# Kernel tuning notes

Measured on AMD Instinct MI355X. Metric: run time of the kernel, lower is better.

Reference implementation:

```python
import jax, jax.numpy as jnp
import numpy as np

EPS = 1e-8  # matches F.cosine_similarity default eps


def setup_inputs() -> dict:
    key = jax.random.key(0)
    k1, k2, k3 = jax.random.split(key, 3)
    B, C, H, W = 16, 256, 64, 64
    n_e = 1024
    z = jax.random.normal(k1, (B, C, H, W), dtype=jnp.float32)
    gt = jax.random.normal(k2, (B, C, H, W), dtype=jnp.float32)
    codebook = jax.random.normal(k3, (n_e, C), dtype=jnp.float32)
    return {"z": z, "gt": gt, "codebook": codebook}


def _sq_dist(x, cb):
    return (jnp.sum(x * x, axis=1, keepdims=True)
            + jnp.sum(cb * cb, axis=1)
            - 2.0 * x @ cb.T)


def reference(z, gt, codebook):
    B, C, H, W = z.shape
    # permute to (B,H,W,C) then flatten to (N, e_dim)
    zf = jnp.transpose(z, (0, 2, 3, 1)).reshape(-1, C)
    gf = jnp.transpose(gt, (0, 2, 3, 1)).reshape(-1, C)

    idx = jnp.argmin(_sq_dist(zf, codebook), axis=1)       # [N]
    idx_gt = jnp.argmin(_sq_dist(gf, codebook), axis=1)    # [N]

    # one-hot @ codebook == direct gather
    z_q = codebook[idx].reshape(B, H, W, C)
    z_q_gt = codebook[idx_gt].reshape(B, H, W, C)

    # F.cosine_similarity(z_q_gt, z_q, dim=1) on (B,H,W,C): reduces over H -> (B,W,C)
    num = jnp.sum(z_q_gt * z_q, axis=1)
    nx = jnp.maximum(jnp.sqrt(jnp.sum(z_q_gt * z_q_gt, axis=1)), EPS)
    ny = jnp.maximum(jnp.sqrt(jnp.sum(z_q * z_q, axis=1)), EPS)
    cosine_score = num / (nx * ny)                         # (B, W, C)

    return cosine_score, idx_gt[:, None], idx[:, None]
```

## Files before the change

### kernel.cpp

```cpp
#include <hip/hip_runtime.h>

typedef _Float16 f16x8 __attribute__((ext_vector_type(8)));
typedef float f32x16 __attribute__((ext_vector_type(16)));

#define CDIM 256
#define NE 1024
#define HW 4096
#define CHW 1048576
#define OUT_COS 262144
#define N_PIX 65536
#define NT 32
#define TAU 0.1f


__global__ void prep_kernel(const float* __restrict__ cb,
                            _Float16* __restrict__ hi,
                            float* __restrict__ c2f,
                            double* __restrict__ c2d) {
    int code = blockIdx.x;
    int lane = threadIdx.x;
    int t = code >> 5, n = code & 31;
    const float* row = cb + code * CDIM;
    double s = 0.0;
    #pragma unroll
    for (int i = 0; i < 4; ++i) {
        int d = i * 64 + lane;
        float x = row[d];
        s += (double)x * (double)x;
        int f = d >> 4, q = (d >> 3) & 1, rr = d & 7;
        hi[(size_t)t * 8192 + f * 512 + q * 256 + n * 8 + rr] = (_Float16)x;
    }
    #pragma unroll
    for (int off = 32; off > 0; off >>= 1)
        s += __shfl_down(s, off, 64);
    if (lane == 0) { c2f[code] = (float)(0.5 * s); c2d[code] = 0.5 * s; }
}

__device__ __forceinline__ void gl_lds16(const _Float16* g, _Float16* l) {
    __builtin_amdgcn_global_load_lds(
        (const __attribute__((address_space(1))) unsigned int*)g,
        (__attribute__((address_space(3))) unsigned int*)l, 16, 0, 0);
}

__launch_bounds__(256, 2)
__global__ void argmin_kernel(const float* __restrict__ Z,
                              const float* __restrict__ GT,
                              const _Float16* __restrict__ ghi,
                              const float* __restrict__ cb,
                              const float* __restrict__ c2f,
                              const double* __restrict__ c2d,
                              float* __restrict__ out_z,
                              float* __restrict__ out_gt) {
    __shared__ __align__(16) _Float16 lbuf[2][8192];
    __shared__ int cand_lds[4][64];
    const int wave = threadIdx.x >> 6;
    const int lane = threadIdx.x & 63;
    const int l31 = lane & 31;
    const int qh = lane >> 5;
    const int half = blockIdx.x >> 8;
    const float* X = half ? GT : Z;
    float* out_idx = half ? out_gt : out_z;
    const int p0 = (blockIdx.x & 255) * 256;

    f16x8 nah[2][16];
    #pragma unroll
    for (int g = 0; g < 2; ++g) {
        const int p = p0 + wave * 64 + g * 32 + l31;
        const float* xbase = X + (size_t)(p >> 12) * CHW + (p & 4095);
        #pragma unroll
        for (int f = 0; f < 16; ++f) {
            #pragma unroll
            for (int j = 0; j < 8; ++j) {
                int d = f * 16 + qh * 8 + j;
                nah[g][f][j] = -(_Float16)xbase[(size_t)d * HW];
            }
        }
    }

    int b1[2][16], b2[2][16];
    #pragma unroll
    for (int g = 0; g < 2; ++g)
        #pragma unroll
        for (int r = 0; r < 16; ++r) { b1[g][r] = 0x7fffffff; b2[g][r] = 0x7fffffff; }

    auto stage = [&](int b, int t) {
        #pragma unroll
        for (int i = 0; i < 4; ++i) {
            const int f = wave * 4 + i;
            gl_lds16(ghi + (size_t)t * 8192 + f * 512 + lane * 8, &lbuf[b][f * 512]);
        }
    };

    stage(0, 0);
    __syncthreads();

    for (int t = 0; t < NT; ++t) {
        const int cur = t & 1;
        if (t < NT - 1) stage(cur ^ 1, t + 1);

        const float c2 = c2f[t * 32 + l31];
        f32x16 acc0, acc1;
        #pragma unroll
        for (int r = 0; r < 16; ++r) { acc0[r] = c2; acc1[r] = c2; }

        #pragma unroll
        for (int f = 0; f < 16; ++f) {
            f16x8 bh = *(const f16x8*)&lbuf[cur][f * 512 + lane * 8];
            acc0 = __builtin_amdgcn_mfma_f32_32x32x16_f16(nah[0][f], bh, acc0, 0, 0, 0);
            acc1 = __builtin_amdgcn_mfma_f32_32x32x16_f16(nah[1][f], bh, acc1, 0, 0, 0);
        }

        const int n = t * 32 + l31;
        #pragma unroll
        for (int r = 0; r < 16; ++r) {
            int k0 = (__float_as_int(acc0[r]) & 0xFFFFFC00) | n;
            int t0 = max(b1[0][r], k0);
            b2[0][r] = min(b2[0][r], t0);
            b1[0][r] = min(b1[0][r], k0);
            int k1 = (__float_as_int(acc1[r]) & 0xFFFFFC00) | n;
            int t1 = max(b1[1][r], k1);
            b2[1][r] = min(b2[1][r], t1);
            b1[1][r] = min(b1[1][r], k1);
        }
        __syncthreads();
    }

    #pragma unroll
    for (int g = 0; g < 2; ++g) {
        #pragma unroll
        for (int r = 0; r < 16; ++r) {
            int x1 = b1[g][r], x2 = b2[g][r];
            #pragma unroll
            for (int off = 16; off > 0; off >>= 1) {
                int o1 = __shfl_xor(x1, off, 64);
                int o2 = __shfl_xor(x2, off, 64);
                int tt = max(x1, o1);
                x2 = min(min(x2, o2), tt);
                x1 = min(x1, o1);
            }
            if (l31 == 0) {
                const int i1 = x1 & 1023, i2 = x2 & 1023;
                const float s1 = __int_as_float(x1 & 0xFFFFFC00);
                const float s2 = __int_as_float(x2 & 0xFFFFFC00);
                const int row = (r & 3) + 8 * (r >> 2) + 4 * qh;
                const int slot = g * 32 + row;
                const bool flag = (s2 - s1) < TAU;
                cand_lds[wave][slot] = i1 | (i2 << 10) | (flag ? (1 << 20) : 0);
                if (!flag) out_idx[p0 + wave * 64 + slot] = (float)i1;
            }
        }
    }

    const int info = cand_lds[wave][lane];
    if (info & (1 << 20)) {
        const int i1 = info & 1023, i2 = (info >> 10) & 1023;
        const int p = p0 + wave * 64 + lane;
        const float* xb = X + (size_t)(p >> 12) * CHW + (p & 4095);
        const float* r1 = cb + (size_t)i1 * CDIM;
        const float* r2 = cb + (size_t)i2 * CDIM;
        double d1 = 0.0, d2 = 0.0;
        #pragma unroll 4
        for (int d = 0; d < CDIM; d += 4) {
            float x0 = xb[(size_t)(d + 0) * HW];
            float x1v = xb[(size_t)(d + 1) * HW];
            float x2v = xb[(size_t)(d + 2) * HW];
            float x3v = xb[(size_t)(d + 3) * HW];
            const float4 v1 = *(const float4*)(r1 + d);
            const float4 v2 = *(const float4*)(r2 + d);
            d1 += (double)x0 * v1.x + (double)x1v * v1.y
                + (double)x2v * v1.z + (double)x3v * v1.w;
            d2 += (double)x0 * v2.x + (double)x1v * v2.y
                + (double)x2v * v2.z + (double)x3v * v2.w;
        }
        const double dd1 = c2d[i1] - d1;
        const double dd2 = c2d[i2] - d2;
        const int bi = (dd2 < dd1 || (dd2 == dd1 && i2 < i1)) ? i2 : i1;
        out_idx[p] = (float)bi;
    }
}

__global__ void cosine_kernel(const float* __restrict__ cb,
                              const float* __restrict__ idx_z_f,
                              const float* __restrict__ idx_gt_f,
                              float* __restrict__ out_cos) {
    __shared__ int s_ig[64], s_iq[64];
    const int bw = blockIdx.x;
    const int c = threadIdx.x;
    const int b = bw >> 6, w = bw & 63;
    if (c < 64) {
        s_ig[c] = (int)idx_gt_f[b * 4096 + c * 64 + w];
    } else if (c < 128) {
        int h = c - 64;
        s_iq[h] = (int)idx_z_f[b * 4096 + h * 64 + w];
    }
    __syncthreads();
    float num = 0.f, sa = 0.f, sb = 0.f;
    #pragma unroll 1
    for (int h = 0; h < 64; h += 4) {
        float av[4], bv[4];
        #pragma unroll
        for (int u = 0; u < 4; ++u) {
            av[u] = cb[s_ig[h + u] * CDIM + c];
            bv[u] = cb[s_iq[h + u] * CDIM + c];
        }
        #pragma unroll
        for (int u = 0; u < 4; ++u) {
            num += av[u] * bv[u];
            sa += av[u] * av[u];
            sb += bv[u] * bv[u];
        }
    }
    const float nx = fmaxf(sqrtf(sa), 1e-8f);
    const float ny = fmaxf(sqrtf(sb), 1e-8f);
    out_cos[bw * CDIM + c] = num / (nx * ny);
}

extern "C" void kernel_launch(void* const* d_in, const int* in_sizes, int n_in,
                              void* d_out, int out_size, void* d_ws, size_t ws_size,
                              hipStream_t stream) {
    const float* z  = (const float*)d_in[0];
    const float* gt = (const float*)d_in[1];
    const float* cb = (const float*)d_in[2];
    float* out = (float*)d_out;

    _Float16* hi = (_Float16*)d_ws;
    float*  c2f = (float*)((char*)d_ws + 512 * 1024);
    double* c2d = (double*)((char*)d_ws + 516 * 1024);

    float* out_cos    = out;
    float* out_idx_gt = out + OUT_COS;
    float* out_idx_z  = out + OUT_COS + N_PIX;

    prep_kernel<<<NE, 64, 0, stream>>>(cb, hi, c2f, c2d);
    argmin_kernel<<<512, 256, 0, stream>>>(z, gt, hi, cb, c2f, c2d,
                                           out_idx_z, out_idx_gt);
    cosine_kernel<<<1024, 256, 0, stream>>>(cb, out_idx_z, out_idx_gt, out_cos);
}
```

Measured before the change: 283.9 us.

## Switch argmin GEMM from 32x32x16 to 16x16x32 MFMA tiles

Replaces the 32x32x16 f16 MFMA with the 16x16x32 variant. Each wave now computes four 16-pixel row groups against two 16-code sub-tiles per 32-code step, and the prep kernel's codebook layout and the final top-2 reduction are changed to match. The goal is to shrink the per-wave accumulator from 32 to 16 floats and the running top-2 state from 64 to 32 registers, easing register pressure and making the argmin update cheaper. In exchange it issues more MFMA instructions and more LDS B-fragment reads per tile.

```diff
diff --git a/kernel.cpp b/kernel.cpp
--- a/kernel.cpp
+++ b/kernel.cpp
@@ -1,7 +1,7 @@
 #include <hip/hip_runtime.h>
 
 typedef _Float16 f16x8 __attribute__((ext_vector_type(8)));
-typedef float f32x16 __attribute__((ext_vector_type(16)));
+typedef float f32x4 __attribute__((ext_vector_type(4)));
 
 #define CDIM 256
 #define NE 1024
@@ -19,7 +19,7 @@
                             double* __restrict__ c2d) {
     int code = blockIdx.x;
     int lane = threadIdx.x;
-    int t = code >> 5, n = code & 31;
+    int t = code >> 5, sub = (code >> 4) & 1, n = code & 15;
     const float* row = cb + code * CDIM;
     double s = 0.0;
     #pragma unroll
@@ -27,8 +27,9 @@
         int d = i * 64 + lane;
         float x = row[d];
         s += (double)x * (double)x;
-        int f = d >> 4, q = (d >> 3) & 1, rr = d & 7;
-        hi[(size_t)t * 8192 + f * 512 + q * 256 + n * 8 + rr] = (_Float16)x;
+        int f = d >> 5, q = (d >> 3) & 3, r = d & 7;
+        hi[(size_t)t * 8192 + sub * 4096 + f * 512 + q * 128 + n * 8 + r] =
+            (_Float16)x;
     }
     #pragma unroll
     for (int off = 32; off > 0; off >>= 1)
@@ -55,39 +56,39 @@
     __shared__ int cand_lds[4][64];
     const int wave = threadIdx.x >> 6;
     const int lane = threadIdx.x & 63;
-    const int l31 = lane & 31;
-    const int qh = lane >> 5;
+    const int l15 = lane & 15;
+    const int quad = lane >> 4;
     const int half = blockIdx.x >> 8;
     const float* X = half ? GT : Z;
     float* out_idx = half ? out_gt : out_z;
     const int p0 = (blockIdx.x & 255) * 256;
 
-    f16x8 nah[2][16];
-    #pragma unroll
-    for (int g = 0; g < 2; ++g) {
-        const int p = p0 + wave * 64 + g * 32 + l31;
+    f16x8 nah[4][8];
+    #pragma unroll
+    for (int g = 0; g < 4; ++g) {
+        const int p = p0 + wave * 64 + g * 16 + l15;
         const float* xbase = X + (size_t)(p >> 12) * CHW + (p & 4095);
         #pragma unroll
-        for (int f = 0; f < 16; ++f) {
+        for (int f = 0; f < 8; ++f) {
             #pragma unroll
             for (int j = 0; j < 8; ++j) {
-                int d = f * 16 + qh * 8 + j;
+                int d = f * 32 + quad * 8 + j;
                 nah[g][f][j] = -(_Float16)xbase[(size_t)d * HW];
             }
         }
     }
 
-    int b1[2][16], b2[2][16];
-    #pragma unroll
-    for (int g = 0; g < 2; ++g)
-        #pragma unroll
-        for (int r = 0; r < 16; ++r) { b1[g][r] = 0x7fffffff; b2[g][r] = 0x7fffffff; }
+    int b1[4][4], b2[4][4];
+    #pragma unroll
+    for (int g = 0; g < 4; ++g)
+        #pragma unroll
+        for (int r = 0; r < 4; ++r) { b1[g][r] = 0x7fffffff; b2[g][r] = 0x7fffffff; }
 
     auto stage = [&](int b, int t) {
         #pragma unroll
         for (int i = 0; i < 4; ++i) {
-            const int f = wave * 4 + i;
-            gl_lds16(ghi + (size_t)t * 8192 + f * 512 + lane * 8, &lbuf[b][f * 512]);
+            const int c = wave * 4 + i;
+            gl_lds16(ghi + (size_t)t * 8192 + c * 512 + lane * 8, &lbuf[b][c * 512]);
         }
     };
 
@@ -98,52 +99,57 @@
         const int cur = t & 1;
         if (t < NT - 1) stage(cur ^ 1, t + 1);
 
-        const float c2 = c2f[t * 32 + l31];
-        f32x16 acc0, acc1;
-        #pragma unroll
-        for (int r = 0; r < 16; ++r) { acc0[r] = c2; acc1[r] = c2; }
-
-        #pragma unroll
-        for (int f = 0; f < 16; ++f) {
-            f16x8 bh = *(const f16x8*)&lbuf[cur][f * 512 + lane * 8];
-            acc0 = __builtin_amdgcn_mfma_f32_32x32x16_f16(nah[0][f], bh, acc0, 0, 0, 0);
-            acc1 = __builtin_amdgcn_mfma_f32_32x32x16_f16(nah[1][f], bh, acc1, 0, 0, 0);
-        }
-
-        const int n = t * 32 + l31;
-        #pragma unroll
-        for (int r = 0; r < 16; ++r) {
-            int k0 = (__float_as_int(acc0[r]) & 0xFFFFFC00) | n;
-            int t0 = max(b1[0][r], k0);
-            b2[0][r] = min(b2[0][r], t0);
-            b1[0][r] = min(b1[0][r], k0);
-            int k1 = (__float_as_int(acc1[r]) & 0xFFFFFC00) | n;
-            int t1 = max(b1[1][r], k1);
-            b2[1][r] = min(b2[1][r], t1);
-            b1[1][r] = min(b1[1][r], k1);
+        #pragma unroll
+        for (int sub = 0; sub < 2; ++sub) {
+            const int n = t * 32 + sub * 16 + l15;
+            const float c2 = c2f[n];
+            f32x4 acc[4];
+            #pragma unroll
+            for (int g = 0; g < 4; ++g)
+                acc[g] = (f32x4){c2, c2, c2, c2};
+
+            #pragma unroll
+            for (int f = 0; f < 8; ++f) {
+                f16x8 bh = *(const f16x8*)&lbuf[cur][sub * 4096 + f * 512 + lane * 8];
+                acc[0] = __builtin_amdgcn_mfma_f32_16x16x32_f16(nah[0][f], bh, acc[0], 0, 0, 0);
+                acc[1] = __builtin_amdgcn_mfma_f32_16x16x32_f16(nah[1][f], bh, acc[1], 0, 0, 0);
+                acc[2] = __builtin_amdgcn_mfma_f32_16x16x32_f16(nah[2][f], bh, acc[2], 0, 0, 0);
+                acc[3] = __builtin_amdgcn_mfma_f32_16x16x32_f16(nah[3][f], bh, acc[3], 0, 0, 0);
+            }
+
+            #pragma unroll
+            for (int g = 0; g < 4; ++g) {
+                #pragma unroll
+                for (int r = 0; r < 4; ++r) {
+                    int k = (__float_as_int(acc[g][r]) & 0xFFFFFC00) | n;
+                    int mx = max(b1[g][r], k);
+                    b2[g][r] = min(b2[g][r], mx);
+                    b1[g][r] = min(b1[g][r], k);
+                }
+            }
         }
         __syncthreads();
     }
 
     #pragma unroll
-    for (int g = 0; g < 2; ++g) {
-        #pragma unroll
-        for (int r = 0; r < 16; ++r) {
+    for (int g = 0; g < 4; ++g) {
+        #pragma unroll
+        for (int r = 0; r < 4; ++r) {
             int x1 = b1[g][r], x2 = b2[g][r];
             #pragma unroll
-            for (int off = 16; off > 0; off >>= 1) {
+            for (int off = 8; off > 0; off >>= 1) {
                 int o1 = __shfl_xor(x1, off, 64);
                 int o2 = __shfl_xor(x2, off, 64);
                 int tt = max(x1, o1);
                 x2 = min(min(x2, o2), tt);
                 x1 = min(x1, o1);
             }
-            if (l31 == 0) {
+            if (l15 == 0) {
                 const int i1 = x1 & 1023, i2 = x2 & 1023;
                 const float s1 = __int_as_float(x1 & 0xFFFFFC00);
                 const float s2 = __int_as_float(x2 & 0xFFFFFC00);
-                const int row = (r & 3) + 8 * (r >> 2) + 4 * qh;
-                const int slot = g * 32 + row;
+                const int row = quad * 4 + r;
+                const int slot = g * 16 + row;
                 const bool flag = (s2 - s1) < TAU;
                 cand_lds[wave][slot] = i1 | (i2 << 10) | (flag ? (1 << 20) : 0);
                 if (!flag) out_idx[p0 + wave * 64 + slot] = (float)i1;
```

Measured after the change: 251.0 us. -11.6%, faster.
